# Performance work log

Measured on AMD Instinct MI355X. Metric: run time of the kernel, lower is better.

Reference implementation:

```python
import jax, jax.numpy as jnp
import numpy as np
from jax import lax

# ---- config (mirrors cfg.* used by the module) ----
ANCHOR_RATIOS = (0.5, 1.0, 2.0)
ANCHOR_SCALES = (8.0, 16.0, 32.0)
FEATURE_STRIDE = 16
BASE_SIZE = 40  # generate_anchors(40, ...)
BN_EPS = 1e-5
LOG_CLAMP = 1e-30  # torch uses 1e-300, which underflows to 0 in fp32; use fp32-safe tiny


def generate_anchors(base_size=BASE_SIZE, ratios=ANCHOR_RATIOS, scales=ANCHOR_SCALES):
    """py-faster-rcnn style anchor generation, corner format (x1,y1,x2,y2). -> (A,4)"""
    w = h = float(base_size)
    cx = (base_size - 1) * 0.5
    cy = (base_size - 1) * 0.5
    size = w * h
    out = []
    for r in ratios:
        ws = np.round(np.sqrt(size / r))
        hs = np.round(ws * r)
        for s in scales:
            W, H = ws * s, hs * s
            out.append([cx - 0.5 * (W - 1), cy - 0.5 * (H - 1),
                        cx + 0.5 * (W - 1), cy + 0.5 * (H - 1)])
    return np.asarray(out, dtype=np.float32)  # (A,4)


def splash_anchors(fH, fW, n, base_anchors, stride):
    """Shift base anchors over the feature grid. -> (n, fH*fW*A, 4), row-major H,W then A."""
    sx = jnp.arange(fW, dtype=jnp.float32) * stride
    sy = jnp.arange(fH, dtype=jnp.float32) * stride
    SY, SX = jnp.meshgrid(sy, sx, indexing='ij')            # (fH,fW)
    shifts = jnp.stack([SX, SY, SX, SY], axis=-1).reshape(-1, 1, 4)  # (fH*fW,1,4)
    anc = (shifts + jnp.asarray(base_anchors)[None, :, :]).reshape(-1, 4)  # (fH*fW*A,4)
    return jnp.broadcast_to(anc[None], (n, anc.shape[0], 4))


def conv2d(x, w, b, pad):
    y = lax.conv_general_dilated(x, w, (1, 1), [(pad, pad), (pad, pad)],
                                 dimension_numbers=('NCHW', 'OIHW', 'NCHW'))
    return y + b[None, :, None, None]


def batchnorm_train(x, gamma, beta):
    # training-mode BN: per-channel batch stats over (N,H,W), biased variance
    m = jnp.mean(x, axis=(0, 2, 3), keepdims=True)
    v = jnp.mean(jnp.square(x - m), axis=(0, 2, 3), keepdims=True)
    xn = (x - m) * lax.rsqrt(v + BN_EPS)
    return xn * gamma[None, :, None, None] + beta[None, :, None, None]


def mish(x):
    return x * jnp.tanh(jax.nn.softplus(x))


def corner2center(b):
    w = b[..., 2] - b[..., 0]
    h = b[..., 3] - b[..., 1]
    cx = b[..., 0] + 0.5 * w
    cy = b[..., 1] + 0.5 * h
    return jnp.stack([cx, cy, w, h], axis=-1)


def setup_inputs() -> dict:
    key = jax.random.key(0)
    ks = jax.random.split(key, 7)
    C_IN, C_BASE, A = 256, 256, 9
    x = jax.random.normal(ks[0], (8, C_IN, 128, 128), dtype=jnp.float32)
    # kaiming-uniform-ish scaled weights
    def kaiming(k, shape):
        fan_in = shape[1] * shape[2] * shape[3]
        bound = float(np.sqrt(6.0 / fan_in))
        return jax.random.uniform(k, shape, jnp.float32, -bound, bound)
    return {
        "x": x,
        "W_base": kaiming(ks[1], (C_BASE, C_IN, 3, 3)),
        "b_base": jnp.zeros((C_BASE,), jnp.float32),
        "g_base": jnp.ones((C_BASE,), jnp.float32),
        "be_base": jnp.zeros((C_BASE,), jnp.float32),
        "W_cls": kaiming(ks[2], (2 * A, C_BASE, 1, 1)),
        "b_cls": jnp.zeros((2 * A,), jnp.float32),
        "g_cls": jnp.ones((2 * A,), jnp.float32),
        "be_cls": jnp.zeros((2 * A,), jnp.float32),
        "W_reg": kaiming(ks[3], (4 * A, C_BASE, 1, 1)),
        "b_reg": jnp.zeros((4 * A,), jnp.float32),
        "g_reg": jnp.ones((4 * A,), jnp.float32),
        "be_reg": jnp.zeros((4 * A,), jnp.float32),
        "img_size": 2048,
    }


def reference(x, W_base, b_base, g_base, be_base,
              W_cls, b_cls, g_cls, be_cls,
              W_reg, b_reg, g_reg, be_reg, img_size):
    n, c, fH, fW = x.shape
    A = 9
    # BASE_CONV: Conv3x3 -> Mish -> Dropout2d (identity here, deterministic) -> BN
    base = batchnorm_train(mish(conv2d(x, W_base, b_base, 1)), g_base, be_base)

    anchors = splash_anchors(fH, fW, n, generate_anchors(), FEATURE_STRIDE)  # (n,K,4) corners

    rpn_reg = batchnorm_train(conv2d(base, W_reg, b_reg, 0), g_reg, be_reg)
    rpn_reg = jnp.transpose(rpn_reg, (0, 2, 3, 1)).reshape(n, -1, 4)          # (n,K,4)

    rpn_score = batchnorm_train(conv2d(base, W_cls, b_cls, 0), g_cls, be_cls)
    rpn_score = jnp.transpose(rpn_score, (0, 2, 3, 1)).reshape(n, fH, fW, A, 2)
    fg_scores = jax.nn.softmax(rpn_score, axis=4)[..., 1].reshape(n, -1)      # (n,K)

    rpn_reg = rpn_reg + anchors                                               # decoded corners

    # proposal layer: clip proposals to the image, keep all (fixed-shape)
    lim = jnp.float32(img_size)
    rois = jnp.clip(rpn_reg, 0.0, lim)                                        # (n,K,4) corners
    rois = corner2center(rois)                                                # (cx,cy,w,h)

    anc_c = corner2center(anchors)
    tx = (rois[..., 0] - anc_c[..., 0]) / anc_c[..., 2]
    ty = (rois[..., 1] - anc_c[..., 1]) / anc_c[..., 3]
    tw = jnp.log(jnp.maximum(rois[..., 2] / anc_c[..., 2], LOG_CLAMP))
    th = jnp.log(jnp.maximum(rois[..., 3] / anc_c[..., 3], LOG_CLAMP))
    ts = jnp.stack([tx, ty, tw, th], axis=-1)
    return (fg_scores, ts, rois)
```

## Files before the change

### kernel.cpp

```cpp
#include <hip/hip_runtime.h>
#include <stdint.h>

typedef short bf16x8 __attribute__((ext_vector_type(8)));
typedef float f32x4 __attribute__((ext_vector_type(4)));

#define AS1 __attribute__((address_space(1)))
#define AS3 __attribute__((address_space(3)))

static __device__ __forceinline__ void gl16(const void* g, void* l) {
  __builtin_amdgcn_global_load_lds((const AS1 void*)g, (AS3 void*)l, 16, 0, 0);
}

static __device__ __forceinline__ unsigned short f2bf(float f) {
  unsigned u = __float_as_uint(f);
  u = u + 0x7fffu + ((u >> 16) & 1u);
  return (unsigned short)(u >> 16);
}
static __device__ __forceinline__ float bf2f(unsigned short h) {
  return __uint_as_float(((unsigned)h) << 16);
}
static __device__ __forceinline__ float mishf(float x) {
  float sp = fmaxf(x, 0.f) + log1pf(expf(-fabsf(x)));
  float e2 = expf(-2.f * sp);
  float th = (1.f - e2) / (1.f + e2);
  return x * th;
}

#define NIMG 8
#define HH 128
#define WW 128
#define HP 130
#define CIN 256
#define MPIX (NIMG * HH * WW)
#define KTOT 2304
#define FGCNT (MPIX * 9)
#define TSCNT (MPIX * 9 * 4)

__device__ __constant__ float AW[9] = {456.f, 912.f, 1824.f, 320.f, 640.f, 1280.f, 224.f, 448.f, 896.f};
__device__ __constant__ float AH[9] = {224.f, 448.f, 896.f, 320.f, 640.f, 1280.f, 448.f, 896.f, 1792.f};

__global__ __launch_bounds__(256) void k_wt(const float* __restrict__ Wb,
                                            unsigned short* __restrict__ Wt2) {
  int d = blockIdx.x * 256 + threadIdx.x;
  int c = d & 31, oc = (d >> 5) & 255, s = d >> 13;
  int kh = s / 24, r = s % 24, kw = r >> 3, icb = r & 7;
  int ic = icb * 32 + c;
  Wt2[d] = f2bf(Wb[((oc * 256 + ic) * 3 + kh) * 3 + kw]);
}

__global__ __launch_bounds__(256) void k_tr(const float* __restrict__ x,
                                            unsigned short* __restrict__ xt2) {
  __shared__ float tile[32][129];
  int b = blockIdx.x;
  int icb = b & 7, h = (b >> 3) & 127, n = b >> 10;
  int t = threadIdx.x;
  const float* src = x + (((size_t)(n * 256 + icb * 32) * 128 + h) * 128);
#pragma unroll
  for (int i = 0; i < 4; ++i) {
    int idx = t + 256 * i;
    int w4 = idx & 31, ic = idx >> 5;
    float4 v = *(const float4*)(src + (size_t)ic * 16384 + w4 * 4);
    tile[ic][w4 * 4 + 0] = v.x; tile[ic][w4 * 4 + 1] = v.y;
    tile[ic][w4 * 4 + 2] = v.z; tile[ic][w4 * 4 + 3] = v.w;
  }
  __syncthreads();
#pragma unroll
  for (int i = 0; i < 8; ++i) {
    int idx = t + 256 * i;
    int icp = idx & 15, w = idx >> 4;
    unsigned lo = f2bf(tile[icp * 2][w]);
    unsigned hi = f2bf(tile[icp * 2 + 1][w]);
    size_t pix = ((size_t)(icb * 8 + n) * HP + (h + 1)) * HP + (w + 1);
    *(unsigned*)(xt2 + pix * 32 + icp * 2) = lo | (hi << 16);
  }
}

__global__ __launch_bounds__(256) void k_bord(unsigned short* __restrict__ xt2) {
  int tid = blockIdx.x * 256 + threadIdx.x;
  int chunk = tid & 3, pix = tid >> 2;
  int nn = pix / 516, bp = pix % 516;
  int hp, wp;
  if (bp < 130) { hp = 0; wp = bp; }
  else if (bp < 260) { hp = 129; wp = bp - 130; }
  else { int r = bp - 260; hp = 1 + (r >> 1); wp = (r & 1) ? 129 : 0; }
  size_t off = (((size_t)nn * HP + hp) * HP + wp) * 32 + chunk * 8;
  uint4 z = {0u, 0u, 0u, 0u};
  *(uint4*)(xt2 + off) = z;
}

__global__ __launch_bounds__(256) void k_conv(const unsigned short* __restrict__ xt2,
                                              const unsigned short* __restrict__ Wt2,
                                              const float* __restrict__ b_base,
                                              unsigned short* __restrict__ yt2,
                                              float* __restrict__ statsA) {
  __shared__ __align__(16) char lds[32768];
  int t = threadIdx.x;
  int lane = t & 63, w4 = t >> 6;
  int wr = w4 >> 1, wc = w4 & 1;
  int row16 = lane & 15, kgl = lane >> 4;
  int pr = lane & 15, pq = lane >> 4;

  int bid = blockIdx.x;
  int swz = (bid & 7) * 256 + (bid >> 3);
  int pixb = swz >> 1, oh = swz & 1;
  int n = pixb >> 7, h0 = pixb & 127;
  size_t M0 = (size_t)pixb * 128;

  f32x4 acc[4][4];
#pragma unroll
  for (int m = 0; m < 4; ++m)
#pragma unroll
    for (int nf = 0; nf < 4; ++nf) { f32x4 z = {0.f, 0.f, 0.f, 0.f}; acc[m][nf] = z; }

  const unsigned short* aS0 =
      xt2 + ((size_t)(n * HP + h0) * HP + w4 * 32 + pr) * 32 + pq * 8;
  const unsigned short* aS1 = aS0 + 16 * 32;
  const unsigned short* bS0 = Wt2 + (size_t)(oh * 128 + w4 * 32 + pr) * 32 + pq * 8;
  const unsigned short* bS1 = bS0 + 16 * 32;

  const size_t planeStride = (size_t)8 * HP * HP * 32;
  int aoffA = wr * 4096 + kgl * 256 + row16 * 16;
  int aoffB = wc * 4096 + kgl * 256 + row16 * 16;

  auto STAGE = [&](int sv, int c_) {
    int icb_ = sv & 7;
    int khw = sv >> 3;
    int kh_ = khw / 3;
    int kw_ = khw - kh_ * 3;
    size_t offA = (size_t)icb_ * planeStride + ((size_t)kh_ * HP + kw_) * 32;
    size_t offB = (size_t)sv * 8192;
    char* buf = lds + c_ * 16384;
    gl16(aS0 + offA, buf + (2 * w4) * 1024);
    gl16(aS1 + offA, buf + (2 * w4 + 1) * 1024);
    gl16(bS0 + offB, buf + 8192 + (2 * w4) * 1024);
    gl16(bS1 + offB, buf + 8192 + (2 * w4 + 1) * 1024);
  };

  STAGE(0, 0);
  int cur = 0;
  for (int s = 0; s < 72; ++s) {
    __syncthreads();
    if (s < 71) STAGE(s + 1, cur ^ 1);
    const char* ab = lds + cur * 16384;
    const char* bb = ab + 8192;
    bf16x8 af[4], bfr[4];
#pragma unroll
    for (int m = 0; m < 4; ++m) af[m] = *(const bf16x8*)(ab + aoffA + m * 1024);
#pragma unroll
    for (int nf = 0; nf < 4; ++nf) bfr[nf] = *(const bf16x8*)(bb + aoffB + nf * 1024);
#pragma unroll
    for (int m = 0; m < 4; ++m)
#pragma unroll
      for (int nf = 0; nf < 4; ++nf)
        acc[m][nf] = __builtin_amdgcn_mfma_f32_16x16x32_bf16(af[m], bfr[nf], acc[m][nf], 0, 0, 0);
    cur ^= 1;
  }

  float sums[4] = {0.f, 0.f, 0.f, 0.f}, sumq[4] = {0.f, 0.f, 0.f, 0.f};
#pragma unroll
  for (int nf = 0; nf < 4; ++nf) {
    int oc = oh * 128 + wc * 64 + nf * 16 + row16;
    float bias = b_base[oc];
    size_t obase = (size_t)(oc >> 5) * MPIX * 32 + (oc & 31);
#pragma unroll
    for (int m = 0; m < 4; ++m) {
#pragma unroll
      for (int j = 0; j < 4; ++j) {
        int p = wr * 64 + m * 16 + kgl * 4 + j;
        float y = mishf(acc[m][nf][j] + bias);
        yt2[obase + (M0 + p) * 32] = f2bf(y);
        sums[nf] += y; sumq[nf] += y * y;
      }
    }
  }
#pragma unroll
  for (int nf = 0; nf < 4; ++nf) {
    float s1 = sums[nf], s2 = sumq[nf];
    s1 += __shfl_xor(s1, 16); s2 += __shfl_xor(s2, 16);
    s1 += __shfl_xor(s1, 32); s2 += __shfl_xor(s2, 32);
    if (lane < 16) {
      int oc = oh * 128 + wc * 64 + nf * 16 + lane;
      atomicAdd(&statsA[oc], s1);
      atomicAdd(&statsA[256 + oc], s2);
    }
  }
}

__global__ __launch_bounds__(256) void k_fold(const float* __restrict__ statsA,
                                              const float* __restrict__ g_base,
                                              const float* __restrict__ be_base,
                                              const float* __restrict__ W_cls,
                                              const float* __restrict__ b_cls,
                                              const float* __restrict__ W_reg,
                                              const float* __restrict__ b_reg,
                                              unsigned short* __restrict__ W2t2,
                                              float* __restrict__ b2) {
  __shared__ float sS[256], sT[256];
  int t = threadIdx.x;
  {
    float cnt = (float)MPIX;
    float m = statsA[t] / cnt;
    float v = fmaxf(statsA[256 + t] / cnt - m * m, 0.f);
    float s = g_base[t] * rsqrtf(v + 1e-5f);
    sS[t] = s;
    sT[t] = be_base[t] - m * s;
  }
  __syncthreads();
  if (t < 64) {
    float bias = 0.f;
    if (t < 36) bias = b_reg[t];
    else if (t < 54) bias = b_cls[t - 36];
    float acc = 0.f;
    for (int ic = 0; ic < 256; ++ic) {
      float w = 0.f;
      if (t < 36) w = W_reg[t * 256 + ic];
      else if (t < 54) w = W_cls[(t - 36) * 256 + ic];
      acc += w * sT[ic];
      W2t2[((size_t)(ic >> 5) * 64 + t) * 32 + (ic & 31)] = f2bf(w * sS[ic]);
    }
    b2[t] = bias + acc;
  }
}

__global__ __launch_bounds__(256) void k_mm2(const unsigned short* __restrict__ yt2,
                                             const unsigned short* __restrict__ W2t2,
                                             const float* __restrict__ b2,
                                             unsigned short* __restrict__ zt,
                                             float* __restrict__ statsZ) {
  __shared__ __align__(16) char lds2[24576];
  int t = threadIdx.x, lane = t & 63, w4 = t >> 6;
  int row16 = lane & 15, kgl = lane >> 4;
  int pr = lane & 15, pq = lane >> 4;
  size_t pixbase = (size_t)blockIdx.x * 128;

  f32x4 acc[2][4];
#pragma unroll
  for (int m = 0; m < 2; ++m)
#pragma unroll
    for (int nn = 0; nn < 4; ++nn) { f32x4 z = {0.f, 0.f, 0.f, 0.f}; acc[m][nn] = z; }

  const unsigned short* aS0 = yt2 + (pixbase + w4 * 32 + pr) * 32 + pq * 8;
  const unsigned short* aS1 = aS0 + 16 * 32;
  const unsigned short* bS = W2t2 + (size_t)(w4 * 16 + pr) * 32 + pq * 8;

  int aoffA = w4 * 2048 + kgl * 256 + row16 * 16;
  int aoffB = kgl * 256 + row16 * 16;

  auto STG = [&](int s, int c_) {
    size_t ao = (size_t)s * MPIX * 32;
    size_t bo = (size_t)s * 2048;
    char* buf = lds2 + c_ * 12288;
    gl16(aS0 + ao, buf + (2 * w4) * 1024);
    gl16(aS1 + ao, buf + (2 * w4 + 1) * 1024);
    gl16(bS + bo, buf + 8192 + w4 * 1024);
  };

  STG(0, 0);
  int cur = 0;
  for (int s = 0; s < 8; ++s) {
    __syncthreads();
    if (s < 7) STG(s + 1, cur ^ 1);
    const char* ab = lds2 + cur * 12288;
    const char* bb = ab + 8192;
    bf16x8 af[2], bfr[4];
#pragma unroll
    for (int m = 0; m < 2; ++m) af[m] = *(const bf16x8*)(ab + aoffA + m * 1024);
#pragma unroll
    for (int nn = 0; nn < 4; ++nn) bfr[nn] = *(const bf16x8*)(bb + aoffB + nn * 1024);
#pragma unroll
    for (int m = 0; m < 2; ++m)
#pragma unroll
      for (int nn = 0; nn < 4; ++nn)
        acc[m][nn] = __builtin_amdgcn_mfma_f32_16x16x32_bf16(af[m], bfr[nn], acc[m][nn], 0, 0, 0);
    cur ^= 1;
  }

  float sums[4] = {0.f, 0.f, 0.f, 0.f}, sumq[4] = {0.f, 0.f, 0.f, 0.f};
#pragma unroll
  for (int nn = 0; nn < 4; ++nn) {
    int oc = nn * 16 + row16;
    float bias = b2[oc];
#pragma unroll
    for (int m = 0; m < 2; ++m) {
#pragma unroll
      for (int j = 0; j < 4; ++j) {
        int p = w4 * 32 + m * 16 + kgl * 4 + j;
        float v = acc[m][nn][j] + bias;
        zt[(pixbase + p) * 64 + oc] = f2bf(v);
        sums[nn] += v; sumq[nn] += v * v;
      }
    }
  }
#pragma unroll
  for (int nn = 0; nn < 4; ++nn) {
    float s1 = sums[nn], s2 = sumq[nn];
    s1 += __shfl_xor(s1, 16); s2 += __shfl_xor(s2, 16);
    s1 += __shfl_xor(s1, 32); s2 += __shfl_xor(s2, 32);
    if (lane < 16) {
      int oc = nn * 16 + lane;
      atomicAdd(&statsZ[oc], s1);
      atomicAdd(&statsZ[64 + oc], s2);
    }
  }
}

__global__ __launch_bounds__(64) void k_zstat(const float* __restrict__ statsZ,
                                              const float* __restrict__ g_cls,
                                              const float* __restrict__ be_cls,
                                              const float* __restrict__ g_reg,
                                              const float* __restrict__ be_reg,
                                              float* __restrict__ zsc,
                                              float* __restrict__ zsh) {
  int t = threadIdx.x;
  float g = 1.f, be = 0.f;
  if (t < 36) { g = g_reg[t]; be = be_reg[t]; }
  else if (t < 54) { g = g_cls[t - 36]; be = be_cls[t - 36]; }
  float cnt = (float)MPIX;
  float m = statsZ[t] / cnt;
  float v = fmaxf(statsZ[64 + t] / cnt - m * m, 0.f);
  float s = g * rsqrtf(v + 1e-5f);
  zsc[t] = s;
  zsh[t] = be - m * s;
}

__global__ __launch_bounds__(256) void k_dec(const unsigned short* __restrict__ zt,
                                             const float* __restrict__ zsc,
                                             const float* __restrict__ zsh,
                                             const int* __restrict__ imgsz,
                                             float* __restrict__ out) {
  int p = blockIdx.x * 256 + threadIdx.x;
  float lim = (float)imgsz[0];
  float zn[64];
  {
    const uint4* zp4 = (const uint4*)(zt + (size_t)p * 64);
#pragma unroll
    for (int i = 0; i < 8; ++i) {
      uint4 v = zp4[i];
      unsigned a0 = v.x, a1 = v.y, a2 = v.z, a3 = v.w;
      zn[i * 8 + 0] = bf2f((unsigned short)(a0 & 0xffff));
      zn[i * 8 + 1] = bf2f((unsigned short)(a0 >> 16));
      zn[i * 8 + 2] = bf2f((unsigned short)(a1 & 0xffff));
      zn[i * 8 + 3] = bf2f((unsigned short)(a1 >> 16));
      zn[i * 8 + 4] = bf2f((unsigned short)(a2 & 0xffff));
      zn[i * 8 + 5] = bf2f((unsigned short)(a2 >> 16));
      zn[i * 8 + 6] = bf2f((unsigned short)(a3 & 0xffff));
      zn[i * 8 + 7] = bf2f((unsigned short)(a3 >> 16));
    }
#pragma unroll
    for (int i = 0; i < 54; ++i) zn[i] = zn[i] * zsc[i] + zsh[i];
  }
  int rem = p & 16383, h = rem >> 7, w = rem & 127;
  float fx = 16.f * (float)w, fy = 16.f * (float)h;
  size_t kbase = (size_t)p * 9;
  float* fgout = out;
  float* tsout = out + FGCNT;
  float* roout = out + FGCNT + TSCNT;
#pragma unroll
  for (int a = 0; a < 9; ++a) {
    float x1 = 20.f - 0.5f * AW[a] + fx;
    float y1 = 20.f - 0.5f * AH[a] + fy;
    float x2 = 19.f + 0.5f * AW[a] + fx;
    float y2 = 19.f + 0.5f * AH[a] + fy;
    float cx1 = fminf(fmaxf(x1 + zn[4 * a + 0], 0.f), lim);
    float cy1 = fminf(fmaxf(y1 + zn[4 * a + 1], 0.f), lim);
    float cx2 = fminf(fmaxf(x2 + zn[4 * a + 2], 0.f), lim);
    float cy2 = fminf(fmaxf(y2 + zn[4 * a + 3], 0.f), lim);
    float bw = cx2 - cx1, bh = cy2 - cy1;
    float cx = cx1 + 0.5f * bw, cy = cy1 + 0.5f * bh;
    float aw = AW[a] - 1.f, ah = AH[a] - 1.f;
    float acx = 19.5f + fx, acy = 19.5f + fy;
    float tx = (cx - acx) / aw, ty = (cy - acy) / ah;
    float tw = logf(fmaxf(bw / aw, 1e-30f));
    float th = logf(fmaxf(bh / ah, 1e-30f));
    float s0 = zn[36 + 2 * a], s1 = zn[36 + 2 * a + 1];
    float fg = 1.f / (1.f + expf(s0 - s1));
    fgout[kbase + a] = fg;
    size_t o4 = (kbase + a) * 4;
    tsout[o4 + 0] = tx; tsout[o4 + 1] = ty; tsout[o4 + 2] = tw; tsout[o4 + 3] = th;
    roout[o4 + 0] = cx; roout[o4 + 1] = cy; roout[o4 + 2] = bw; roout[o4 + 3] = bh;
  }
}

extern "C" void kernel_launch(void* const* d_in, const int* in_sizes, int n_in,
                              void* d_out, int out_size, void* d_ws, size_t ws_size,
                              hipStream_t stream) {
  const float* x   = (const float*)d_in[0];
  const float* Wb  = (const float*)d_in[1];
  const float* bb  = (const float*)d_in[2];
  const float* gb  = (const float*)d_in[3];
  const float* beb = (const float*)d_in[4];
  const float* Wc  = (const float*)d_in[5];
  const float* bc  = (const float*)d_in[6];
  const float* gc  = (const float*)d_in[7];
  const float* bec = (const float*)d_in[8];
  const float* Wr  = (const float*)d_in[9];
  const float* br  = (const float*)d_in[10];
  const float* gr  = (const float*)d_in[11];
  const float* ber = (const float*)d_in[12];
  const int* imgsz = (const int*)d_in[13];

  char* ws = (char*)d_ws;
  const size_t OFF_XTP = 0;
  const size_t OFF_Y   = 69222400;
  const size_t OFF_Z   = 136331264;
  const size_t OFF_WT  = 153108480;
  const size_t OFF_W2  = 154288128;
  const size_t OFF_S   = 154320896;
  unsigned short* xt2  = (unsigned short*)(ws + OFF_XTP);
  unsigned short* yt2  = (unsigned short*)(ws + OFF_Y);
  unsigned short* zt   = (unsigned short*)(ws + OFF_Z);
  unsigned short* Wt2  = (unsigned short*)(ws + OFF_WT);
  unsigned short* W2t2 = (unsigned short*)(ws + OFF_W2);
  float* b2     = (float*)(ws + OFF_S);
  float* statsA = (float*)(ws + OFF_S + 256);
  float* statsZ = (float*)(ws + OFF_S + 2304);
  float* zsc    = (float*)(ws + OFF_S + 2816);
  float* zsh    = (float*)(ws + OFF_S + 3072);
  float* out = (float*)d_out;

  hipMemsetAsync(statsA, 0, (512 + 128) * sizeof(float), stream);
  k_wt  <<<2304, 256, 0, stream>>>(Wb, Wt2);
  k_tr  <<<8192, 256, 0, stream>>>(x, xt2);
  k_bord<<<516, 256, 0, stream>>>(xt2);
  k_conv<<<2048, 256, 0, stream>>>(xt2, Wt2, bb, yt2, statsA);
  k_fold<<<1, 256, 0, stream>>>(statsA, gb, beb, Wc, bc, Wr, br, W2t2, b2);
  k_mm2 <<<1024, 256, 0, stream>>>(yt2, W2t2, b2, zt, statsZ);
  k_zstat<<<1, 64, 0, stream>>>(statsZ, gc, bec, gr, ber, zsc, zsh);
  k_dec <<<512, 256, 0, stream>>>(zt, zsc, zsh, imgsz, out);
}
```

Before: 536.1 us.

## Process two K-slices per barrier and reorder K loop to icb-major

The conv GEMM main loop now loads two 32-wide K slices per iteration into single-buffered LDS and runs twice as many MFMAs between barriers, instead of the previous double-buffered one-slice-ahead prefetch. The K ordering changes to input-channel-block major with kh/kw inner, and the weight pre-transpose is updated to match. This halves the iteration and barrier count but drops overlap of global loads with compute, since each iteration waits on its own loads and adds a second barrier.

Result: slower. 594.6 us (+10.9%).

```diff
diff --git a/kernel.cpp b/kernel.cpp
--- a/kernel.cpp
+++ b/kernel.cpp
@@ -43,7 +43,7 @@
                                             unsigned short* __restrict__ Wt2) {
   int d = blockIdx.x * 256 + threadIdx.x;
   int c = d & 31, oc = (d >> 5) & 255, s = d >> 13;
-  int kh = s / 24, r = s % 24, kw = r >> 3, icb = r & 7;
+  int icb = s / 9, khw = s % 9, kh = khw / 3, kw = khw % 3;
   int ic = icb * 32 + c;
   Wt2[d] = f2bf(Wb[((oc * 256 + ic) * 3 + kh) * 3 + kw]);
 }
@@ -122,38 +122,46 @@
   int aoffA = wr * 4096 + kgl * 256 + row16 * 16;
   int aoffB = wc * 4096 + kgl * 256 + row16 * 16;
 
-  auto STAGE = [&](int sv, int c_) {
-    int icb_ = sv & 7;
-    int khw = sv >> 3;
-    int kh_ = khw / 3;
+  auto aoff32 = [&](int sl) -> size_t {
+    int icb_ = (sl * 57) >> 9;
+    int khw = sl - icb_ * 9;
+    int kh_ = (khw * 11) >> 5;
     int kw_ = khw - kh_ * 3;
-    size_t offA = (size_t)icb_ * planeStride + ((size_t)kh_ * HP + kw_) * 32;
-    size_t offB = (size_t)sv * 8192;
-    char* buf = lds + c_ * 16384;
-    gl16(aS0 + offA, buf + (2 * w4) * 1024);
-    gl16(aS1 + offA, buf + (2 * w4 + 1) * 1024);
-    gl16(bS0 + offB, buf + 8192 + (2 * w4) * 1024);
-    gl16(bS1 + offB, buf + 8192 + (2 * w4 + 1) * 1024);
+    return (size_t)icb_ * planeStride + ((size_t)kh_ * HP + kw_) * 32;
   };
 
-  STAGE(0, 0);
-  int cur = 0;
-  for (int s = 0; s < 72; ++s) {
+  for (int s = 0; s < 36; ++s) {
+#pragma unroll
+    for (int kc = 0; kc < 2; ++kc) {
+      int sl = 2 * s + kc;
+      size_t offA = aoff32(sl);
+      size_t offB = (size_t)sl * 8192;
+      char* bufA = lds + kc * 8192;
+      char* bufB = lds + 16384 + kc * 8192;
+      gl16(aS0 + offA, bufA + (2 * w4) * 1024);
+      gl16(aS1 + offA, bufA + (2 * w4 + 1) * 1024);
+      gl16(bS0 + offB, bufB + (2 * w4) * 1024);
+      gl16(bS1 + offB, bufB + (2 * w4 + 1) * 1024);
+    }
     __syncthreads();
-    if (s < 71) STAGE(s + 1, cur ^ 1);
-    const char* ab = lds + cur * 16384;
-    const char* bb = ab + 8192;
-    bf16x8 af[4], bfr[4];
-#pragma unroll
-    for (int m = 0; m < 4; ++m) af[m] = *(const bf16x8*)(ab + aoffA + m * 1024);
-#pragma unroll
-    for (int nf = 0; nf < 4; ++nf) bfr[nf] = *(const bf16x8*)(bb + aoffB + nf * 1024);
+    bf16x8 af[4][2], bfr[4][2];
+#pragma unroll
+    for (int kc = 0; kc < 2; ++kc) {
+#pragma unroll
+      for (int m = 0; m < 4; ++m)
+        af[m][kc] = *(const bf16x8*)(lds + kc * 8192 + aoffA + m * 1024);
+#pragma unroll
+      for (int nf = 0; nf < 4; ++nf)
+        bfr[nf][kc] = *(const bf16x8*)(lds + 16384 + kc * 8192 + aoffB + nf * 1024);
+    }
 #pragma unroll
     for (int m = 0; m < 4; ++m)
 #pragma unroll
-      for (int nf = 0; nf < 4; ++nf)
-        acc[m][nf] = __builtin_amdgcn_mfma_f32_16x16x32_bf16(af[m], bfr[nf], acc[m][nf], 0, 0, 0);
-    cur ^= 1;
+      for (int nf = 0; nf < 4; ++nf) {
+        acc[m][nf] = __builtin_amdgcn_mfma_f32_16x16x32_bf16(af[m][0], bfr[nf][0], acc[m][nf], 0, 0, 0);
+        acc[m][nf] = __builtin_amdgcn_mfma_f32_16x16x32_bf16(af[m][1], bfr[nf][1], acc[m][nf], 0, 0, 0);
+      }
+    __syncthreads();
   }
 
   float sums[4] = {0.f, 0.f, 0.f, 0.f}, sumq[4] = {0.f, 0.f, 0.f, 0.f};
```
